# Performance work log

Measured on AMD Instinct MI355X. Metric: run time of the kernel, lower is better.

Reference implementation:

```python
import jax, jax.numpy as jnp
import numpy as np

K = 2          # top-k experts kept (init kwarg k)
TEMP = 1.0     # gating temperature


def setup_inputs() -> dict:
    key = jax.random.key(0)
    ks = jax.random.split(key, 5)
    B, S, D, O, E = 4, 2048, 1024, 1024, 8
    scale = 1.0 / np.sqrt(D)
    x = jax.random.normal(ks[0], (B, S, D), dtype=jnp.float32)
    W = jax.random.normal(ks[1], (E, O, D), dtype=jnp.float32) * scale   # per-expert Linear weight [out,in]
    b = jax.random.normal(ks[2], (E, O), dtype=jnp.float32) * 0.01
    Wg = jax.random.normal(ks[3], (E, D), dtype=jnp.float32) * scale     # gate Linear weight [E,in]
    bg = jnp.zeros((E,), dtype=jnp.float32)
    return {"x": x, "W": W, "b": b, "Wg": Wg, "bg": bg}


def reference(x, W, b, Wg, bg):
    # gating: softmax over experts (per token, segment_expert_trigger=False)
    gate_logits = (jnp.einsum('bsd,ed->bse', x, Wg) + bg) / TEMP
    gate_scores = jax.nn.softmax(gate_logits, axis=-1)                   # [B,S,E]
    topk_scores, topk_idx = jax.lax.top_k(gate_scores, K)                # [B,S,K]
    # dense all-expert projection (matches torch.stack of per-expert Linear)
    expert_outputs = jnp.einsum('bsd,eod->bseo', x, W) + b               # [B,S,E,O]
    # gather the top-k expert outputs, scale by gate score, and sum
    selected = jnp.take_along_axis(expert_outputs, topk_idx[..., None], axis=2)  # [B,S,K,O]
    output = jnp.sum(selected * topk_scores[..., None], axis=2)          # [B,S,O]
    return output
```

## Files before the change

kernel.cpp:

```cpp
#include <hip/hip_runtime.h>
#include <hip/hip_bf16.h>

#define NTOK 8192
#define DDIM 1024
#define ODIM 1024
#define NEXP 8
#define BK   32
#define NKT  (DDIM / BK)

typedef __attribute__((ext_vector_type(8))) short short8;
typedef __attribute__((ext_vector_type(4))) float f32x4;

#define CNT_OFF   0u
#define SC_OFF    (4u * 1024u)
#define LIST_OFF  (128u * 1024u)
#define XH_OFF    (1u << 20)
#define WH_OFF    ((1u << 20) + 16u*1024u*1024u)
#define O2_OFF    ((1u << 20) + 32u*1024u*1024u)
#define WS_NEED   ((size_t)O2_OFF + (size_t)NTOK * ODIM * 4u)

__device__ inline unsigned short f2bf(float f) {
    unsigned int u = __float_as_uint(f);
    unsigned int r = (u + 0x7FFFu + ((u >> 16) & 1u)) >> 16;
    return (unsigned short)r;
}

__device__ inline void glds16(const unsigned short* g, unsigned short* l) {
    __builtin_amdgcn_global_load_lds(
        (const __attribute__((address_space(1))) unsigned int*)g,
        (__attribute__((address_space(3))) unsigned int*)l, 16, 0, 0);
}

__global__ void k_cvtw(const float4* __restrict__ src, ushort4* __restrict__ dst,
                       int n4, int* __restrict__ counts) {
    if (blockIdx.x == 0 && threadIdx.x < 16) counts[threadIdx.x] = 0;
    int i = blockIdx.x * blockDim.x + threadIdx.x;
    if (i >= n4) return;
    float4 v = src[i];
    ushort4 o;
    o.x = f2bf(v.x); o.y = f2bf(v.y); o.z = f2bf(v.z); o.w = f2bf(v.w);
    dst[i] = o;
}

__global__ __launch_bounds__(256) void k_gate(
    const float* __restrict__ x, const float* __restrict__ Wg,
    const float* __restrict__ bg, float* __restrict__ scores2,
    int* __restrict__ lists, int* __restrict__ counts,
    unsigned short* __restrict__ xh)
{
    __shared__ unsigned char s_eid[16];
    const int tid = threadIdx.x, wave = tid >> 6, lane = tid & 63;
    const int tblk = blockIdx.x * 8;

    #pragma unroll 1
    for (int ti = 0; ti < 2; ti++) {
        const int t = tblk + wave * 2 + ti;
        const float* xr = x + (size_t)t * DDIM;
        float4 xv[4];
        #pragma unroll
        for (int i = 0; i < 4; i++)
            xv[i] = *(const float4*)&xr[lane * 4 + 256 * i];

        unsigned short* xhr = xh + (size_t)t * DDIM;
        #pragma unroll
        for (int i = 0; i < 4; i++) {
            ushort4 h;
            h.x = f2bf(xv[i].x); h.y = f2bf(xv[i].y);
            h.z = f2bf(xv[i].z); h.w = f2bf(xv[i].w);
            *(ushort4*)&xhr[lane * 4 + 256 * i] = h;
        }

        double lg[NEXP];
        #pragma unroll
        for (int e = 0; e < NEXP; e++) {
            const float* wr = Wg + (size_t)e * DDIM;
            double a = 0.0;
            #pragma unroll
            for (int i = 0; i < 4; i++) {
                float4 wv = *(const float4*)&wr[lane * 4 + 256 * i];
                a += (double)xv[i].x * (double)wv.x + (double)xv[i].y * (double)wv.y
                   + (double)xv[i].z * (double)wv.z + (double)xv[i].w * (double)wv.w;
            }
            #pragma unroll
            for (int off = 32; off > 0; off >>= 1) a += __shfl_xor(a, off);
            lg[e] = a + (double)bg[e];
        }

        int i0 = -1, i1 = -1;
        double best = -1e300, sec = -1e300;
        #pragma unroll
        for (int e = 0; e < NEXP; e++) {
            double v = lg[e];
            if (v > best) { sec = best; i1 = i0; best = v; i0 = e; }
            else if (v > sec) { sec = v; i1 = e; }
        }
        float sum = 0.f;
        #pragma unroll
        for (int e = 0; e < NEXP; e++) sum += expf((float)(lg[e] - best));
        float s0 = 1.f / sum;
        float s1 = expf((float)(sec - best)) / sum;

        if (lane == 0) {
            scores2[t * 2 + 0] = s0;
            scores2[t * 2 + 1] = s1;
            int le = (wave * 2 + ti) * 2;
            s_eid[le + 0] = (unsigned char)i0;
            s_eid[le + 1] = (unsigned char)i1;
        }
    }
    __syncthreads();

    if (tid < 16) {
        int e = tid & 7, kk = tid >> 3;
        int c = 0;
        #pragma unroll
        for (int j = 0; j < 8; j++) c += (s_eid[j * 2 + kk] == e);
        if (c) {
            int p = atomicAdd(&counts[tid], c);
            #pragma unroll
            for (int j = 0; j < 8; j++)
                if (s_eid[j * 2 + kk] == e)
                    lists[tid * NTOK + (p++)] = (tblk + j) * 2 + kk;
        }
    }
}

__global__ __launch_bounds__(256, 4) void k_gemm(
    const unsigned short* __restrict__ xh, const unsigned short* __restrict__ wh,
    const int* __restrict__ counts, const int* __restrict__ lists,
    const float* __restrict__ scores2, const float* __restrict__ bias,
    float* __restrict__ out, float* __restrict__ out2, int listLo, int listHi)
{
    __shared__ __align__(16) unsigned short As[2][128 * BK];
    __shared__ __align__(16) unsigned short Bs[2][128 * BK];

    const int nwg = (int)gridDim.x;
    const int bid0 = ((int)blockIdx.x & 7) * (nwg >> 3) + ((int)blockIdx.x >> 3);
    const int tid = threadIdx.x, wid = tid >> 6, lane = tid & 63;

    int cnts[16];
    #pragma unroll
    for (int i = 0; i < 16; i++) cnts[i] = counts[i];
    int tbLo = 0, tbHi = 0;
    #pragma unroll
    for (int i = 0; i < 16; i++) {
        int nt_ = ((cnts[i] + 127) >> 7) * 8;
        if (i < listLo) tbLo += nt_;
        if (i < listHi) tbHi += nt_;
    }

    const int rl = lane >> 2;
    const int wm = wid >> 1, wn = wid & 1;
    const int fr = lane & 15, g4 = lane >> 4;

    #pragma unroll 1
    for (int tile = tbLo + bid0; tile < tbHi; tile += nwg) {
        int li = 0, base = 0, cnt = 0, acc_ = 0;
        #pragma unroll
        for (int i = 0; i < 16; i++) {
            int nt_ = ((cnts[i] + 127) >> 7) * 8;
            if (tile >= acc_) { li = i; base = acc_; cnt = cnts[i]; }
            acc_ += nt_;
        }
        const int local = tile - base, mt = local >> 3, ntc = local & 7;
        const int m0 = mt * 128, n0 = ntc * 128;
        const int* list = lists + li * NTOK;
        const int exp_ = li & 7;
        const unsigned short* whE = wh + (size_t)exp_ * ODIM * DDIM;

        const unsigned short* aS[2];
        const unsigned short* bS[2];
        int rb[2];
        #pragma unroll
        for (int i = 0; i < 2; i++) {
            int R = wid * 32 + i * 16 + rl;
            int sl = (lane & 3) ^ ((R >> 1) & 3);
            int g = m0 + R; if (g >= cnt) g = cnt - 1;
            aS[i] = xh + (size_t)(list[g] >> 1) * DDIM + sl * 8;
            bS[i] = whE + (size_t)(n0 + R) * DDIM + sl * 8;
            rb[i] = (wid * 32 + i * 16) * BK;
        }

        f32x4 acc[4][4];
        #pragma unroll
        for (int m = 0; m < 4; m++)
            #pragma unroll
            for (int n = 0; n < 4; n++)
                acc[m][n] = (f32x4){0.f, 0.f, 0.f, 0.f};

        #pragma unroll
        for (int i = 0; i < 2; i++) {
            glds16(aS[i], &As[0][rb[i]]);
            glds16(bS[i], &Bs[0][rb[i]]);
        }

        int buf = 0;
        #pragma unroll 1
        for (int t = 0; t < NKT; t++) {
            __syncthreads();
            if (t + 1 < NKT) {
                const int k0 = (t + 1) * BK;
                #pragma unroll
                for (int i = 0; i < 2; i++) {
                    glds16(aS[i] + k0, &As[buf ^ 1][rb[i]]);
                    glds16(bS[i] + k0, &Bs[buf ^ 1][rb[i]]);
                }
            }
            short8 af[4], bf_[4];
            #pragma unroll
            for (int m = 0; m < 4; m++) {
                int R = wm * 64 + m * 16 + fr;
                int ph = g4 ^ ((R >> 1) & 3);
                af[m] = *(const short8*)&As[buf][R * BK + ph * 8];
            }
            #pragma unroll
            for (int n = 0; n < 4; n++) {
                int R = wn * 64 + n * 16 + fr;
                int ph = g4 ^ ((R >> 1) & 3);
                bf_[n] = *(const short8*)&Bs[buf][R * BK + ph * 8];
            }
            #pragma unroll
            for (int m = 0; m < 4; m++)
                #pragma unroll
                for (int n = 0; n < 4; n++)
                    acc[m][n] = __builtin_amdgcn_mfma_f32_16x16x32_bf16(
                        af[m], bf_[n], acc[m][n], 0, 0, 0);
            buf ^= 1;
        }

        const bool rank1 = (li >= 8);
        float* dstBase = (rank1 && out2 != nullptr) ? out2 : out;
        const bool rmw = rank1 && (out2 == nullptr);
        const float* brow = bias + (size_t)exp_ * ODIM + n0 + wn * 64 + fr;
        float bv[4];
        #pragma unroll
        for (int n = 0; n < 4; n++) bv[n] = brow[n * 16];

        #pragma unroll
        for (int m = 0; m < 4; m++) {
            #pragma unroll
            for (int j = 0; j < 4; j++) {
                int r = wm * 64 + m * 16 + g4 * 4 + j;
                int gr = m0 + r;
                if (gr < cnt) {
                    int entry = list[gr];
                    float s = scores2[entry];
                    float* orow = dstBase + (size_t)(entry >> 1) * ODIM + n0 + wn * 64 + fr;
                    if (rmw) {
                        #pragma unroll
                        for (int n = 0; n < 4; n++)
                            orow[n * 16] += s * (acc[m][n][j] + bv[n]);
                    } else {
                        #pragma unroll
                        for (int n = 0; n < 4; n++)
                            orow[n * 16] = s * (acc[m][n][j] + bv[n]);
                    }
                }
            }
        }
    }
}

__global__ void k_add(float4* __restrict__ out, const float4* __restrict__ out2, int n4) {
    int i = blockIdx.x * blockDim.x + threadIdx.x;
    const int stride = gridDim.x * blockDim.x;
    #pragma unroll 1
    for (; i < n4; i += stride) {
        float4 a = out[i], c = out2[i];
        a.x += c.x; a.y += c.y; a.z += c.z; a.w += c.w;
        out[i] = a;
    }
}

extern "C" void kernel_launch(void* const* d_in, const int* in_sizes, int n_in,
                              void* d_out, int out_size, void* d_ws, size_t ws_size,
                              hipStream_t stream) {
    const float* x  = (const float*)d_in[0];
    const float* W  = (const float*)d_in[1];
    const float* b  = (const float*)d_in[2];
    const float* Wg = (const float*)d_in[3];
    const float* bg = (const float*)d_in[4];
    float* out = (float*)d_out;
    char* ws = (char*)d_ws;

    int*   counts  = (int*)(ws + CNT_OFF);
    float* scores2 = (float*)(ws + SC_OFF);
    int*   lists   = (int*)(ws + LIST_OFF);
    unsigned short* xh = (unsigned short*)(ws + XH_OFF);
    unsigned short* wh = (unsigned short*)(ws + WH_OFF);
    float* out2 = (float*)(ws + O2_OFF);

    int n4w = NEXP * ODIM * DDIM / 4;
    k_cvtw<<<n4w / 256, 256, 0, stream>>>((const float4*)W, (ushort4*)wh, n4w, counts);

    k_gate<<<NTOK / 8, 256, 0, stream>>>(x, Wg, bg, scores2, lists, counts, xh);

    if (ws_size >= WS_NEED) {
        k_gemm<<<1024, 256, 0, stream>>>(xh, wh, counts, lists, scores2, b, out, out2, 0, 16);
        k_add<<<2048, 256, 0, stream>>>((float4*)out, (const float4*)out2, NTOK * ODIM / 4);
    } else {
        k_gemm<<<1024, 256, 0, stream>>>(xh, wh, counts, lists, scores2, b, out, nullptr, 0, 8);
        k_gemm<<<1024, 256, 0, stream>>>(xh, wh, counts, lists, scores2, b, out, nullptr, 8, 16);
    }
}
```

Before: 140.4 us.

## Widen GEMM tile to 128x256 and map one tile per block

The expert GEMM tile grows from 128x128 to 128x256. Each wave now covers all 128 rows and a 64-column slice, holding 8x4 MFMA accumulators. The persistent tile loop is replaced by a one-tile-per-block mapping, with a grid of 576 sized to the worst-case tile count, and the occupancy hint in launch_bounds is dropped. The aim is to halve repeated A-tile (gathered token) loads and cut per-tile scheduling overhead. In exchange, registers and LDS per block rise, which lowers occupancy, and fewer, larger blocks may leave a load-imbalanced tail across CUs.

After: 189.0 us. 1.35x slower.

```diff
diff --git a/kernel.cpp b/kernel.cpp
--- a/kernel.cpp
+++ b/kernel.cpp
@@ -125,136 +125,125 @@
     }
 }
 
-__global__ __launch_bounds__(256, 4) void k_gemm(
+__global__ __launch_bounds__(256) void k_gemm(
     const unsigned short* __restrict__ xh, const unsigned short* __restrict__ wh,
     const int* __restrict__ counts, const int* __restrict__ lists,
     const float* __restrict__ scores2, const float* __restrict__ bias,
     float* __restrict__ out, float* __restrict__ out2, int listLo, int listHi)
 {
     __shared__ __align__(16) unsigned short As[2][128 * BK];
-    __shared__ __align__(16) unsigned short Bs[2][128 * BK];
+    __shared__ __align__(16) unsigned short Bs[2][256 * BK];
 
     const int nwg = (int)gridDim.x;
-    const int bid0 = ((int)blockIdx.x & 7) * (nwg >> 3) + ((int)blockIdx.x >> 3);
+    int bid = ((int)blockIdx.x & 7) * (nwg >> 3) + ((int)blockIdx.x >> 3);
+
+    int li = -1, mt = 0, nt = 0, cnt = 0;
+    #pragma unroll
+    for (int i = 0; i < 16; i++) {
+        if (i < listLo || i >= listHi) continue;
+        int c = counts[i];
+        int tiles = ((c + 127) >> 7) * 4;
+        if (li < 0) {
+            if (bid < tiles) { li = i; mt = bid >> 2; nt = bid & 3; cnt = c; }
+            else bid -= tiles;
+        }
+    }
+    if (li < 0) return;
+
+    const int m0 = mt * 128, n0 = nt * 256;
+    const int* list = lists + li * NTOK;
+    const int exp_ = li & 7;
+    const unsigned short* whE = wh + (size_t)exp_ * ODIM * DDIM;
     const int tid = threadIdx.x, wid = tid >> 6, lane = tid & 63;
 
-    int cnts[16];
-    #pragma unroll
-    for (int i = 0; i < 16; i++) cnts[i] = counts[i];
-    int tbLo = 0, tbHi = 0;
-    #pragma unroll
-    for (int i = 0; i < 16; i++) {
-        int nt_ = ((cnts[i] + 127) >> 7) * 8;
-        if (i < listLo) tbLo += nt_;
-        if (i < listHi) tbHi += nt_;
-    }
-
-    const int rl = lane >> 2;
-    const int wm = wid >> 1, wn = wid & 1;
+    const int rl = lane >> 2, slx = lane & 3;
+    const unsigned short* aS[2];
+    const unsigned short* bS[4];
+    int rbA[2], rbB[4];
+    #pragma unroll
+    for (int i = 0; i < 2; i++) {
+        int R = i * 64 + wid * 16 + rl;
+        int sl = slx ^ ((R >> 1) & 3);
+        int g = m0 + R; if (g >= cnt) g = cnt - 1;
+        aS[i] = xh + (size_t)(list[g] >> 1) * DDIM + sl * 8;
+        rbA[i] = (i * 64 + wid * 16) * BK;
+    }
+    #pragma unroll
+    for (int c = 0; c < 4; c++) {
+        int R = c * 64 + wid * 16 + rl;
+        int sl = slx ^ ((R >> 1) & 3);
+        bS[c] = whE + (size_t)(n0 + R) * DDIM + sl * 8;
+        rbB[c] = (c * 64 + wid * 16) * BK;
+    }
+
     const int fr = lane & 15, g4 = lane >> 4;
-
+    const int ph = g4 ^ ((fr >> 1) & 3);
+
+    f32x4 acc[8][4];
+    #pragma unroll
+    for (int m = 0; m < 8; m++)
+        #pragma unroll
+        for (int n = 0; n < 4; n++)
+            acc[m][n] = (f32x4){0.f, 0.f, 0.f, 0.f};
+
+    #pragma unroll
+    for (int i = 0; i < 2; i++) glds16(aS[i], &As[0][rbA[i]]);
+    #pragma unroll
+    for (int c = 0; c < 4; c++) glds16(bS[c], &Bs[0][rbB[c]]);
+
+    int buf = 0;
     #pragma unroll 1
-    for (int tile = tbLo + bid0; tile < tbHi; tile += nwg) {
-        int li = 0, base = 0, cnt = 0, acc_ = 0;
-        #pragma unroll
-        for (int i = 0; i < 16; i++) {
-            int nt_ = ((cnts[i] + 127) >> 7) * 8;
-            if (tile >= acc_) { li = i; base = acc_; cnt = cnts[i]; }
-            acc_ += nt_;
-        }
-        const int local = tile - base, mt = local >> 3, ntc = local & 7;
-        const int m0 = mt * 128, n0 = ntc * 128;
-        const int* list = lists + li * NTOK;
-        const int exp_ = li & 7;
-        const unsigned short* whE = wh + (size_t)exp_ * ODIM * DDIM;
-
-        const unsigned short* aS[2];
-        const unsigned short* bS[2];
-        int rb[2];
-        #pragma unroll
-        for (int i = 0; i < 2; i++) {
-            int R = wid * 32 + i * 16 + rl;
-            int sl = (lane & 3) ^ ((R >> 1) & 3);
-            int g = m0 + R; if (g >= cnt) g = cnt - 1;
-            aS[i] = xh + (size_t)(list[g] >> 1) * DDIM + sl * 8;
-            bS[i] = whE + (size_t)(n0 + R) * DDIM + sl * 8;
-            rb[i] = (wid * 32 + i * 16) * BK;
-        }
-
-        f32x4 acc[4][4];
-        #pragma unroll
-        for (int m = 0; m < 4; m++)
+    for (int t = 0; t < NKT; t++) {
+        __syncthreads();
+        if (t + 1 < NKT) {
+            const int k0 = (t + 1) * BK;
+            #pragma unroll
+            for (int i = 0; i < 2; i++) glds16(aS[i] + k0, &As[buf ^ 1][rbA[i]]);
+            #pragma unroll
+            for (int c = 0; c < 4; c++) glds16(bS[c] + k0, &Bs[buf ^ 1][rbB[c]]);
+        }
+        short8 af[8], bf_[4];
+        #pragma unroll
+        for (int m = 0; m < 8; m++)
+            af[m] = *(const short8*)&As[buf][(m * 16 + fr) * BK + ph * 8];
+        #pragma unroll
+        for (int n = 0; n < 4; n++)
+            bf_[n] = *(const short8*)&Bs[buf][(wid * 64 + n * 16 + fr) * BK + ph * 8];
+        #pragma unroll
+        for (int m = 0; m < 8; m++)
             #pragma unroll
             for (int n = 0; n < 4; n++)
-                acc[m][n] = (f32x4){0.f, 0.f, 0.f, 0.f};
-
-        #pragma unroll
-        for (int i = 0; i < 2; i++) {
-            glds16(aS[i], &As[0][rb[i]]);
-            glds16(bS[i], &Bs[0][rb[i]]);
-        }
-
-        int buf = 0;
-        #pragma unroll 1
-        for (int t = 0; t < NKT; t++) {
-            __syncthreads();
-            if (t + 1 < NKT) {
-                const int k0 = (t + 1) * BK;
-                #pragma unroll
-                for (int i = 0; i < 2; i++) {
-                    glds16(aS[i] + k0, &As[buf ^ 1][rb[i]]);
-                    glds16(bS[i] + k0, &Bs[buf ^ 1][rb[i]]);
-                }
-            }
-            short8 af[4], bf_[4];
-            #pragma unroll
-            for (int m = 0; m < 4; m++) {
-                int R = wm * 64 + m * 16 + fr;
-                int ph = g4 ^ ((R >> 1) & 3);
-                af[m] = *(const short8*)&As[buf][R * BK + ph * 8];
-            }
-            #pragma unroll
-            for (int n = 0; n < 4; n++) {
-                int R = wn * 64 + n * 16 + fr;
-                int ph = g4 ^ ((R >> 1) & 3);
-                bf_[n] = *(const short8*)&Bs[buf][R * BK + ph * 8];
-            }
-            #pragma unroll
-            for (int m = 0; m < 4; m++)
-                #pragma unroll
-                for (int n = 0; n < 4; n++)
-                    acc[m][n] = __builtin_amdgcn_mfma_f32_16x16x32_bf16(
-                        af[m], bf_[n], acc[m][n], 0, 0, 0);
-            buf ^= 1;
-        }
-
-        const bool rank1 = (li >= 8);
-        float* dstBase = (rank1 && out2 != nullptr) ? out2 : out;
-        const bool rmw = rank1 && (out2 == nullptr);
-        const float* brow = bias + (size_t)exp_ * ODIM + n0 + wn * 64 + fr;
-        float bv[4];
-        #pragma unroll
-        for (int n = 0; n < 4; n++) bv[n] = brow[n * 16];
-
-        #pragma unroll
-        for (int m = 0; m < 4; m++) {
-            #pragma unroll
-            for (int j = 0; j < 4; j++) {
-                int r = wm * 64 + m * 16 + g4 * 4 + j;
-                int gr = m0 + r;
-                if (gr < cnt) {
-                    int entry = list[gr];
-                    float s = scores2[entry];
-                    float* orow = dstBase + (size_t)(entry >> 1) * ODIM + n0 + wn * 64 + fr;
-                    if (rmw) {
-                        #pragma unroll
-                        for (int n = 0; n < 4; n++)
-                            orow[n * 16] += s * (acc[m][n][j] + bv[n]);
-                    } else {
-                        #pragma unroll
-                        for (int n = 0; n < 4; n++)
-                            orow[n * 16] = s * (acc[m][n][j] + bv[n]);
-                    }
+                acc[m][n] = __builtin_amdgcn_mfma_f32_16x16x32_bf16(
+                    af[m], bf_[n], acc[m][n], 0, 0, 0);
+        buf ^= 1;
+    }
+
+    const bool rank1 = (li >= 8);
+    float* dstBase = (rank1 && out2 != nullptr) ? out2 : out;
+    const bool rmw = rank1 && (out2 == nullptr);
+    const float* brow = bias + (size_t)exp_ * ODIM + n0 + wid * 64 + fr;
+    float bv[4];
+    #pragma unroll
+    for (int n = 0; n < 4; n++) bv[n] = brow[n * 16];
+
+    #pragma unroll
+    for (int m = 0; m < 8; m++) {
+        #pragma unroll
+        for (int j = 0; j < 4; j++) {
+            int r = m * 16 + g4 * 4 + j;
+            int gr = m0 + r;
+            if (gr < cnt) {
+                int entry = list[gr];
+                float s = scores2[entry];
+                float* orow = dstBase + (size_t)(entry >> 1) * ODIM + n0 + wid * 64 + fr;
+                if (rmw) {
+                    #pragma unroll
+                    for (int n = 0; n < 4; n++)
+                        orow[n * 16] += s * (acc[m][n][j] + bv[n]);
+                } else {
+                    #pragma unroll
+                    for (int n = 0; n < 4; n++)
+                        orow[n * 16] = s * (acc[m][n][j] + bv[n]);
                 }
             }
         }
@@ -296,10 +285,10 @@
     k_gate<<<NTOK / 8, 256, 0, stream>>>(x, Wg, bg, scores2, lists, counts, xh);
 
     if (ws_size >= WS_NEED) {
-        k_gemm<<<1024, 256, 0, stream>>>(xh, wh, counts, lists, scores2, b, out, out2, 0, 16);
+        k_gemm<<<576, 256, 0, stream>>>(xh, wh, counts, lists, scores2, b, out, out2, 0, 16);
         k_add<<<2048, 256, 0, stream>>>((float4*)out, (const float4*)out2, NTOK * ODIM / 4);
     } else {
-        k_gemm<<<1024, 256, 0, stream>>>(xh, wh, counts, lists, scores2, b, out, nullptr, 0, 8);
-        k_gemm<<<1024, 256, 0, stream>>>(xh, wh, counts, lists, scores2, b, out, nullptr, 8, 16);
-    }
-}
+        k_gemm<<<576, 256, 0, stream>>>(xh, wh, counts, lists, scores2, b, out, nullptr, 0, 8);
+        k_gemm<<<576, 256, 0, stream>>>(xh, wh, counts, lists, scores2, b, out, nullptr, 8, 16);
+    }
+}
```

## Double GEMM K-tile to 64 and launch one tile per block

Applied to the files above, without the earlier changes.

The routed expert GEMM now loads 64-wide K slices instead of 32. It uses a new XOR swizzle on the LDS layout and issues two MFMA k-steps per barrier, which halves the number of synchronisations per tile. The persistent tile loop is replaced by a grid of 1152 blocks, the worst-case tile count, where each block locates its single tile and exits early if it has none. The min-blocks launch bound is dropped. LDS use doubles to 64KB per block, which may lower occupancy and latency hiding.

After: 146.7 us. +4.5%, slower.

```diff
diff --git a/kernel.cpp b/kernel.cpp
--- a/kernel.cpp
+++ b/kernel.cpp
@@ -5,7 +5,7 @@
 #define DDIM 1024
 #define ODIM 1024
 #define NEXP 8
-#define BK   32
+#define BK   64
 #define NKT  (DDIM / BK)
 
 typedef __attribute__((ext_vector_type(8))) short short8;
@@ -125,7 +125,7 @@
     }
 }
 
-__global__ __launch_bounds__(256, 4) void k_gemm(
+__global__ __launch_bounds__(256) void k_gemm(
     const unsigned short* __restrict__ xh, const unsigned short* __restrict__ wh,
     const int* __restrict__ counts, const int* __restrict__ lists,
     const float* __restrict__ scores2, const float* __restrict__ bias,
@@ -135,126 +135,135 @@
     __shared__ __align__(16) unsigned short Bs[2][128 * BK];
 
     const int nwg = (int)gridDim.x;
-    const int bid0 = ((int)blockIdx.x & 7) * (nwg >> 3) + ((int)blockIdx.x >> 3);
+    int bid = ((int)blockIdx.x & 7) * (nwg >> 3) + ((int)blockIdx.x >> 3);
+
+    int li = -1, mt = 0, nt = 0, cnt = 0;
+    #pragma unroll
+    for (int i = 0; i < 16; i++) {
+        if (i < listLo || i >= listHi) continue;
+        int c = counts[i];
+        int tiles = ((c + 127) >> 7) * 8;
+        if (li < 0) {
+            if (bid < tiles) { li = i; mt = bid >> 3; nt = bid & 7; cnt = c; }
+            else bid -= tiles;
+        }
+    }
+    if (li < 0) return;
+
+    const int m0 = mt * 128, n0 = nt * 128;
+    const int* list = lists + li * NTOK;
+    const int exp_ = li & 7;
+    const unsigned short* whE = wh + (size_t)exp_ * ODIM * DDIM;
     const int tid = threadIdx.x, wid = tid >> 6, lane = tid & 63;
 
-    int cnts[16];
-    #pragma unroll
-    for (int i = 0; i < 16; i++) cnts[i] = counts[i];
-    int tbLo = 0, tbHi = 0;
-    #pragma unroll
-    for (int i = 0; i < 16; i++) {
-        int nt_ = ((cnts[i] + 127) >> 7) * 8;
-        if (i < listLo) tbLo += nt_;
-        if (i < listHi) tbHi += nt_;
-    }
-
-    const int rl = lane >> 2;
+    const int l8 = lane >> 3, s8 = lane & 7;
+    const unsigned short* aS[4];
+    const unsigned short* bS[4];
+    int rbase[4];
+    #pragma unroll
+    for (int i = 0; i < 4; i++) {
+        const int rb = (wid * 4 + i) * 8;
+        rbase[i] = rb;
+        const int P = rb + l8;
+        const int c = s8 ^ (P & 7);
+        int g = m0 + P; if (g >= cnt) g = cnt - 1;
+        aS[i] = xh + (size_t)(list[g] >> 1) * DDIM + c * 8;
+        bS[i] = whE + (size_t)(n0 + P) * DDIM + c * 8;
+    }
+
     const int wm = wid >> 1, wn = wid & 1;
     const int fr = lane & 15, g4 = lane >> 4;
-
+    int offA[4][2], offB[4][2];
+    #pragma unroll
+    for (int m = 0; m < 4; m++) {
+        int R = wm * 64 + m * 16 + fr;
+        #pragma unroll
+        for (int kk = 0; kk < 2; kk++)
+            offA[m][kk] = (R * 128 + kk * 64 + g4 * 16) ^ ((R & 7) << 4);
+    }
+    #pragma unroll
+    for (int n = 0; n < 4; n++) {
+        int R = wn * 64 + n * 16 + fr;
+        #pragma unroll
+        for (int kk = 0; kk < 2; kk++)
+            offB[n][kk] = (R * 128 + kk * 64 + g4 * 16) ^ ((R & 7) << 4);
+    }
+
+    f32x4 acc[4][4];
+    #pragma unroll
+    for (int m = 0; m < 4; m++)
+        #pragma unroll
+        for (int n = 0; n < 4; n++)
+            acc[m][n] = (f32x4){0.f, 0.f, 0.f, 0.f};
+
+    #pragma unroll
+    for (int i = 0; i < 4; i++) {
+        glds16(aS[i], &As[0][rbase[i] * BK]);
+        glds16(bS[i], &Bs[0][rbase[i] * BK]);
+    }
+
+    int buf = 0;
     #pragma unroll 1
-    for (int tile = tbLo + bid0; tile < tbHi; tile += nwg) {
-        int li = 0, base = 0, cnt = 0, acc_ = 0;
-        #pragma unroll
-        for (int i = 0; i < 16; i++) {
-            int nt_ = ((cnts[i] + 127) >> 7) * 8;
-            if (tile >= acc_) { li = i; base = acc_; cnt = cnts[i]; }
-            acc_ += nt_;
-        }
-        const int local = tile - base, mt = local >> 3, ntc = local & 7;
-        const int m0 = mt * 128, n0 = ntc * 128;
-        const int* list = lists + li * NTOK;
-        const int exp_ = li & 7;
-        const unsigned short* whE = wh + (size_t)exp_ * ODIM * DDIM;
-
-        const unsigned short* aS[2];
-        const unsigned short* bS[2];
-        int rb[2];
-        #pragma unroll
-        for (int i = 0; i < 2; i++) {
-            int R = wid * 32 + i * 16 + rl;
-            int sl = (lane & 3) ^ ((R >> 1) & 3);
-            int g = m0 + R; if (g >= cnt) g = cnt - 1;
-            aS[i] = xh + (size_t)(list[g] >> 1) * DDIM + sl * 8;
-            bS[i] = whE + (size_t)(n0 + R) * DDIM + sl * 8;
-            rb[i] = (wid * 32 + i * 16) * BK;
-        }
-
-        f32x4 acc[4][4];
-        #pragma unroll
-        for (int m = 0; m < 4; m++)
-            #pragma unroll
-            for (int n = 0; n < 4; n++)
-                acc[m][n] = (f32x4){0.f, 0.f, 0.f, 0.f};
-
-        #pragma unroll
-        for (int i = 0; i < 2; i++) {
-            glds16(aS[i], &As[0][rb[i]]);
-            glds16(bS[i], &Bs[0][rb[i]]);
-        }
-
-        int buf = 0;
-        #pragma unroll 1
-        for (int t = 0; t < NKT; t++) {
-            __syncthreads();
-            if (t + 1 < NKT) {
-                const int k0 = (t + 1) * BK;
-                #pragma unroll
-                for (int i = 0; i < 2; i++) {
-                    glds16(aS[i] + k0, &As[buf ^ 1][rb[i]]);
-                    glds16(bS[i] + k0, &Bs[buf ^ 1][rb[i]]);
-                }
+    for (int t = 0; t < NKT; t++) {
+        __syncthreads();
+        if (t + 1 < NKT) {
+            const int k0 = (t + 1) * BK;
+            #pragma unroll
+            for (int i = 0; i < 4; i++) {
+                glds16(aS[i] + k0, &As[buf ^ 1][rbase[i] * BK]);
+                glds16(bS[i] + k0, &Bs[buf ^ 1][rbase[i] * BK]);
             }
-            short8 af[4], bf_[4];
-            #pragma unroll
-            for (int m = 0; m < 4; m++) {
-                int R = wm * 64 + m * 16 + fr;
-                int ph = g4 ^ ((R >> 1) & 3);
-                af[m] = *(const short8*)&As[buf][R * BK + ph * 8];
-            }
-            #pragma unroll
-            for (int n = 0; n < 4; n++) {
-                int R = wn * 64 + n * 16 + fr;
-                int ph = g4 ^ ((R >> 1) & 3);
-                bf_[n] = *(const short8*)&Bs[buf][R * BK + ph * 8];
-            }
+        }
+        const char* ab = (const char*)&As[buf][0];
+        const char* bb = (const char*)&Bs[buf][0];
+        short8 af[4][2], bfv[4][2];
+        #pragma unroll
+        for (int m = 0; m < 4; m++) {
+            af[m][0] = *(const short8*)(ab + offA[m][0]);
+            af[m][1] = *(const short8*)(ab + offA[m][1]);
+        }
+        #pragma unroll
+        for (int n = 0; n < 4; n++) {
+            bfv[n][0] = *(const short8*)(bb + offB[n][0]);
+            bfv[n][1] = *(const short8*)(bb + offB[n][1]);
+        }
+        #pragma unroll
+        for (int kk = 0; kk < 2; kk++)
             #pragma unroll
             for (int m = 0; m < 4; m++)
                 #pragma unroll
                 for (int n = 0; n < 4; n++)
                     acc[m][n] = __builtin_amdgcn_mfma_f32_16x16x32_bf16(
-                        af[m], bf_[n], acc[m][n], 0, 0, 0);
-            buf ^= 1;
-        }
-
-        const bool rank1 = (li >= 8);
-        float* dstBase = (rank1 && out2 != nullptr) ? out2 : out;
-        const bool rmw = rank1 && (out2 == nullptr);
-        const float* brow = bias + (size_t)exp_ * ODIM + n0 + wn * 64 + fr;
-        float bv[4];
-        #pragma unroll
-        for (int n = 0; n < 4; n++) bv[n] = brow[n * 16];
-
-        #pragma unroll
-        for (int m = 0; m < 4; m++) {
-            #pragma unroll
-            for (int j = 0; j < 4; j++) {
-                int r = wm * 64 + m * 16 + g4 * 4 + j;
-                int gr = m0 + r;
-                if (gr < cnt) {
-                    int entry = list[gr];
-                    float s = scores2[entry];
-                    float* orow = dstBase + (size_t)(entry >> 1) * ODIM + n0 + wn * 64 + fr;
-                    if (rmw) {
-                        #pragma unroll
-                        for (int n = 0; n < 4; n++)
-                            orow[n * 16] += s * (acc[m][n][j] + bv[n]);
-                    } else {
-                        #pragma unroll
-                        for (int n = 0; n < 4; n++)
-                            orow[n * 16] = s * (acc[m][n][j] + bv[n]);
-                    }
+                        af[m][kk], bfv[n][kk], acc[m][n], 0, 0, 0);
+        buf ^= 1;
+    }
+
+    const bool rank1 = (li >= 8);
+    float* dstBase = (rank1 && out2 != nullptr) ? out2 : out;
+    const bool rmw = rank1 && (out2 == nullptr);
+    const float* brow = bias + (size_t)exp_ * ODIM + n0 + wn * 64 + fr;
+    float bv[4];
+    #pragma unroll
+    for (int n = 0; n < 4; n++) bv[n] = brow[n * 16];
+
+    #pragma unroll
+    for (int m = 0; m < 4; m++) {
+        #pragma unroll
+        for (int j = 0; j < 4; j++) {
+            int r = wm * 64 + m * 16 + g4 * 4 + j;
+            int gr = m0 + r;
+            if (gr < cnt) {
+                int entry = list[gr];
+                float s = scores2[entry];
+                float* orow = dstBase + (size_t)(entry >> 1) * ODIM + n0 + wn * 64 + fr;
+                if (rmw) {
+                    #pragma unroll
+                    for (int n = 0; n < 4; n++)
+                        orow[n * 16] += s * (acc[m][n][j] + bv[n]);
+                } else {
+                    #pragma unroll
+                    for (int n = 0; n < 4; n++)
+                        orow[n * 16] = s * (acc[m][n][j] + bv[n]);
                 }
             }
         }
@@ -296,10 +305,10 @@
     k_gate<<<NTOK / 8, 256, 0, stream>>>(x, Wg, bg, scores2, lists, counts, xh);
 
     if (ws_size >= WS_NEED) {
-        k_gemm<<<1024, 256, 0, stream>>>(xh, wh, counts, lists, scores2, b, out, out2, 0, 16);
+        k_gemm<<<1152, 256, 0, stream>>>(xh, wh, counts, lists, scores2, b, out, out2, 0, 16);
         k_add<<<2048, 256, 0, stream>>>((float4*)out, (const float4*)out2, NTOK * ODIM / 4);
     } else {
-        k_gemm<<<1024, 256, 0, stream>>>(xh, wh, counts, lists, scores2, b, out, nullptr, 0, 8);
-        k_gemm<<<1024, 256, 0, stream>>>(xh, wh, counts, lists, scores2, b, out, nullptr, 8, 16);
-    }
-}
+        k_gemm<<<1152, 256, 0, stream>>>(xh, wh, counts, lists, scores2, b, out, nullptr, 0, 8);
+        k_gemm<<<1152, 256, 0, stream>>>(xh, wh, counts, lists, scores2, b, out, nullptr, 8, 16);
+    }
+}
```
